# Performance work log

Hardware: AMD Instinct MI355X
Metric: run time of the kernel (lower is better)

Reference implementation:

```python
import jax, jax.numpy as jnp
import numpy as np

N = 50000      # nodes
E = 600000     # edges (avg degree 12)
D = 128        # in_dim == hidden_dim
H = 4          # heads
HD = 32        # per-head dim (hidden_dim // heads)
NEG = 0.2      # GATv2 leaky_relu negative slope (PyG default)
EPS = 1e-5     # LayerNorm eps


def setup_inputs() -> dict:
    key = jax.random.key(0)
    ks = jax.random.split(key, 4)
    inp = {
        "x": jax.random.normal(ks[0], (N, D), jnp.float32),
        "edge_index": jax.random.randint(ks[1], (2, E), 0, N, dtype=jnp.int32),
    }
    glorot = 1.0 / np.sqrt(D)
    for i in range(2):
        k = jax.random.split(jax.random.fold_in(ks[2], i), 8)
        inp[f"Wl{i}"] = jax.random.normal(k[0], (D, H * HD), jnp.float32) * glorot
        inp[f"bl{i}"] = jnp.zeros((H * HD,), jnp.float32)
        inp[f"Wr{i}"] = jax.random.normal(k[1], (D, H * HD), jnp.float32) * glorot
        inp[f"br{i}"] = jnp.zeros((H * HD,), jnp.float32)
        inp[f"att{i}"] = jax.random.normal(k[2], (H, HD), jnp.float32) * (1.0 / np.sqrt(HD))
        inp[f"bias{i}"] = jnp.zeros((H * HD,), jnp.float32)
        inp[f"g{i}"] = jnp.ones((H * HD,), jnp.float32)   # LayerNorm gamma
        inp[f"b{i}"] = jnp.zeros((H * HD,), jnp.float32)  # LayerNorm beta
    return inp


def _gat_layer(h, src, dst, Wl, bl, Wr, br, att, bias, g, b):
    # GATv2: x_l from source nodes, x_r from destination nodes
    xl = (h @ Wl + bl).reshape(N, H, HD)
    xr = (h @ Wr + br).reshape(N, H, HD)
    # edge-wise attention score: att . leaky_relu(x_l[j] + x_r[i])
    e = jax.nn.leaky_relu(xl[src] + xr[dst], NEG)          # [E, H, HD]
    score = jnp.einsum('ehd,hd->eh', e, att)               # [E, H]
    # segment softmax over edges sharing a destination
    m = jax.ops.segment_max(score, dst, num_segments=N)    # [N, H]
    m = jnp.where(jnp.isfinite(m), m, 0.0)                 # isolated nodes
    ex = jnp.exp(score - m[dst])
    den = jax.ops.segment_sum(ex, dst, num_segments=N)
    alpha = ex / (den[dst] + 1e-16)                        # [E, H]
    # scatter-add aggregation of source messages
    out = jax.ops.segment_sum(alpha[:, :, None] * xl[src], dst, num_segments=N)
    out = out.reshape(N, H * HD) + bias
    # LayerNorm + ELU (dropout is identity in eval mode)
    mu = out.mean(-1, keepdims=True)
    var = out.var(-1, keepdims=True)
    out = (out - mu) / jnp.sqrt(var + EPS) * g + b
    return jax.nn.elu(out)


def reference(x, edge_index, Wl0, bl0, Wr0, br0, att0, bias0, g0, b0,
              Wl1, bl1, Wr1, br1, att1, bias1, g1, b1):
    src, dst = edge_index[0], edge_index[1]
    h = _gat_layer(x, src, dst, Wl0, bl0, Wr0, br0, att0, bias0, g0, b0)
    h = _gat_layer(h, src, dst, Wl1, bl1, Wr1, br1, att1, bias1, g1, b1)
    return h
```

## Files before the change

### kernel.cpp

```cpp
#include <hip/hip_runtime.h>

#define NN 50000
#define NN_PAD 50016
#define NE 600000
#define DD 128
#define NH 4
#define RB_CNT 3125
#define RB_PAD 3128

#define SCAN_T 512
#define SCAN_B ((NN + SCAN_T - 1) / SCAN_T)

#define LOG2E 1.44269504088896340736f

typedef short s16x8 __attribute__((ext_vector_type(8)));
typedef float f32x4 __attribute__((ext_vector_type(4)));

__device__ __forceinline__ unsigned short bfh(float f) {
  unsigned u = __float_as_uint(f);
  return (unsigned short)((u + 0x7fffu + ((u >> 16) & 1u)) >> 16);
}
__device__ __forceinline__ float bff(unsigned short h) {
  return __uint_as_float(((unsigned)h) << 16);
}

template <int CTRL>
__device__ __forceinline__ float dpp_add(float x) {
  int y = __builtin_amdgcn_update_dpp(0, __float_as_int(x), CTRL, 0xf, 0xf, true);
  return x + __int_as_float(y);
}

__global__ void zero_deg(int* __restrict__ deg) {
  int i = (blockIdx.x * 256 + threadIdx.x) << 2;
  if (i < NN) {
    int4 z = make_int4(0, 0, 0, 0);
    if (i + 3 < NN) *(int4*)(deg + i) = z;
    else for (int k = i; k < NN; k++) deg[k] = 0;
  }
}

__global__ void count_deg(const int* __restrict__ ei, int* __restrict__ deg) {
  int e = blockIdx.x * 256 + threadIdx.x;
  if (e < NE) atomicAdd(deg + ei[NE + e], 1);
}

__global__ __launch_bounds__(SCAN_T) void scan_partial(
    const int* __restrict__ deg, int* __restrict__ rowp, int* __restrict__ bsum) {
  __shared__ int buf[SCAN_T];
  int b = blockIdx.x, t = threadIdx.x;
  int i = b * SCAN_T + t;
  int v = (i < NN) ? deg[i] : 0;
  buf[t] = v;
  __syncthreads();
  for (int o = 1; o < SCAN_T; o <<= 1) {
    int add = (t >= o) ? buf[t - o] : 0;
    __syncthreads();
    buf[t] += add;
    __syncthreads();
  }
  if (i < NN) rowp[i] = buf[t] - v;
  if (t == SCAN_T - 1) bsum[b] = buf[t];
}

__global__ __launch_bounds__(SCAN_T) void scan_finish(
    const int* __restrict__ bsum, int* __restrict__ rowp, int* __restrict__ cur) {
  __shared__ int sb[SCAN_T];
  int b = blockIdx.x, t = threadIdx.x;
  int v = (t < SCAN_B) ? bsum[t] : 0;
  sb[t] = v;
  __syncthreads();
  for (int o = 1; o < SCAN_T; o <<= 1) {
    int add = (t >= o) ? sb[t - o] : 0;
    __syncthreads();
    sb[t] += add;
    __syncthreads();
  }
  int boff = sb[b] - bsum[b];
  int i = b * SCAN_T + t;
  if (i < NN) {
    int r = rowp[i] + boff;
    rowp[i] = r;
    cur[i] = r;
  }
  if (b == 0 && t == 0) rowp[NN] = sb[SCAN_B - 1];
}

__global__ void scatter_src(const int* __restrict__ ei,
                            int* __restrict__ cur, int* __restrict__ colsrc) {
  int e = blockIdx.x * 256 + threadIdx.x;
  if (e < NE) {
    int d = ei[NE + e];
    int p = atomicAdd(cur + d, 1);
    colsrc[p] = ei[e] << 8;
  }
}

__global__ __launch_bounds__(256) void prep_all(
    const float* __restrict__ h,
    const float* __restrict__ Wl0, const float* __restrict__ Wr0,
    const float* __restrict__ Wl1, const float* __restrict__ Wr1,
    unsigned short* __restrict__ Ah, unsigned short* __restrict__ Am,
    unsigned short* __restrict__ Bh, unsigned short* __restrict__ Bm) {
  int b = blockIdx.x;
  if (b < RB_CNT) {
    int tid = b * 256 + threadIdx.x;
    int lr = tid & 15;
    int g = (tid >> 4) & 3;
    int kt = (tid >> 6) & 3;
    int rb = tid >> 8;
    int row = rb * 16 + lr;
    const float* p = h + (size_t)row * DD + kt * 32 + 4 * g;
    float4 f0 = *(const float4*)(p);
    float4 f1 = *(const float4*)(p + 16);
    float fs[8] = {f0.x, f0.y, f0.z, f0.w, f1.x, f1.y, f1.z, f1.w};
    s16x8 hi, mid;
#pragma unroll
    for (int e = 0; e < 8; e++) {
      unsigned short hh = bfh(fs[e]);
      hi[e] = (short)hh;
      mid[e] = (short)bfh(fs[e] - bff(hh));
    }
    *(s16x8*)(Ah + (size_t)tid * 8) = hi;
    *(s16x8*)(Am + (size_t)tid * 8) = mid;
  } else {
    int tid = (b - RB_CNT) * 256 + threadIdx.x;
    int lay = tid >> 12;
    int t = tid & 4095;
    int lr = t & 15;
    int g = (t >> 4) & 3;
    int kt = (t >> 6) & 3;
    int ct = t >> 8;
    int col = ct * 16 + lr;
    const float* W = (col < DD) ? (lay ? Wl1 : Wl0) : (lay ? Wr1 : Wr0);
    int cc = (col < DD) ? col : col - DD;
    s16x8 hi, mid;
#pragma unroll
    for (int e = 0; e < 8; e++) {
      int k = kt * 32 + ((e >> 2) << 4) + 4 * g + (e & 3);
      float w = W[(size_t)k * DD + cc];
      unsigned short hh = bfh(w);
      hi[e] = (short)hh;
      mid[e] = (short)bfh(w - bff(hh));
    }
    *(s16x8*)(Bh + (size_t)tid * 8) = hi;
    *(s16x8*)(Bm + (size_t)tid * 8) = mid;
  }
}

__global__ __launch_bounds__(256, 3) void dual_gemm_mfma(
    const unsigned short* __restrict__ Ah, const unsigned short* __restrict__ Am,
    const unsigned short* __restrict__ Bh, const unsigned short* __restrict__ Bm,
    const float* __restrict__ blv, const float* __restrict__ brv,
    unsigned short* __restrict__ xlb, unsigned short* __restrict__ xrb) {
  const int tid = threadIdx.x;
  const int lane = tid & 63;
  const int wv = tid >> 6;
  const int lr = lane & 15;
  const int g = lane >> 4;
  const int rb0 = blockIdx.x * 2;

  f32x4 acc[2][4];
#pragma unroll
  for (int rt = 0; rt < 2; rt++)
#pragma unroll
    for (int nt = 0; nt < 4; nt++)
#pragma unroll
      for (int e = 0; e < 4; e++) acc[rt][nt][e] = 0.f;

#pragma unroll
  for (int kt = 0; kt < 4; kt++) {
    s16x8 ah[2], am[2], bh[4], bm[4];
#pragma unroll
    for (int rt = 0; rt < 2; rt++) {
      size_t off = ((((size_t)((rb0 + rt) * 4 + kt)) * 4 + g) * 16 + lr) * 8;
      ah[rt] = *(const s16x8*)(Ah + off);
      am[rt] = *(const s16x8*)(Am + off);
    }
#pragma unroll
    for (int nt = 0; nt < 4; nt++) {
      int ct = wv * 4 + nt;
      size_t off = ((((size_t)(ct * 4 + kt)) * 4 + g) * 16 + lr) * 8;
      bh[nt] = *(const s16x8*)(Bh + off);
      bm[nt] = *(const s16x8*)(Bm + off);
    }
#pragma unroll
    for (int rt = 0; rt < 2; rt++)
#pragma unroll
      for (int nt = 0; nt < 4; nt++) {
        acc[rt][nt] = __builtin_amdgcn_mfma_f32_16x16x32_bf16(ah[rt], bh[nt], acc[rt][nt], 0, 0, 0);
        acc[rt][nt] = __builtin_amdgcn_mfma_f32_16x16x32_bf16(ah[rt], bm[nt], acc[rt][nt], 0, 0, 0);
        acc[rt][nt] = __builtin_amdgcn_mfma_f32_16x16x32_bf16(am[rt], bh[nt], acc[rt][nt], 0, 0, 0);
      }
  }

#pragma unroll
  for (int nt = 0; nt < 4; nt++) {
    int col = wv * 64 + nt * 16 + lr;
    unsigned short* dst = (col < DD) ? (xlb + col) : (xrb + (col - DD));
    float bv = (col < DD) ? blv[col] : brv[col - DD];
#pragma unroll
    for (int rt = 0; rt < 2; rt++) {
      int rowb = blockIdx.x * 32 + rt * 16 + 4 * g;
#pragma unroll
      for (int r = 0; r < 4; r++)
        dst[(size_t)(rowb + r) * DD] = bfh(acc[rt][nt][r] + bv);
    }
  }
}

template <int SPLIT>
__global__ __launch_bounds__(256) void fused_edge_agg(
    const int* __restrict__ rowp, const int* __restrict__ colsrc,
    const unsigned short* __restrict__ xlb, const unsigned short* __restrict__ xrb,
    const float* __restrict__ att, const float* __restrict__ bias,
    const float* __restrict__ gam, const float* __restrict__ bet,
    float* __restrict__ out, unsigned short* __restrict__ Oh,
    unsigned short* __restrict__ Om) {
  int node = (blockIdx.x * 256 + threadIdx.x) >> 5;
  if (node >= NN) return;
  int il = threadIdx.x & 31;
  int d0 = il << 2;

  ushort4 xru = *(const ushort4*)(xrb + (size_t)node * DD + d0);
  float4 xrv; xrv.x = bff(xru.x); xrv.y = bff(xru.y);
  xrv.z = bff(xru.z); xrv.w = bff(xru.w);
  float4 atv = *(const float4*)(att + d0);
  atv.x *= LOG2E; atv.y *= LOG2E; atv.z *= LOG2E; atv.w *= LOG2E;
  int j0 = rowp[node];
  int j1 = rowp[node + 1];

  float den = 0.f;
  float a0 = 0.f, a1 = 0.f, a2 = 0.f, a3 = 0.f;
  const char* xlb8 = (const char*)xlb;
  const int goff = il << 3;

  for (int j = j0; j < j1; j += 4) {
    bool v1 = (j + 1) < j1, v2 = (j + 2) < j1, v3 = (j + 3) < j1;
    int s0 = colsrc[j];
    int s1 = colsrc[v1 ? j + 1 : j];
    int s2 = colsrc[v2 ? j + 2 : j];
    int s3 = colsrc[v3 ? j + 3 : j];
    ushort4 g0 = *(const ushort4*)(xlb8 + (size_t)(unsigned)(s0 + goff));
    ushort4 g1 = *(const ushort4*)(xlb8 + (size_t)(unsigned)(s1 + goff));
    ushort4 g2 = *(const ushort4*)(xlb8 + (size_t)(unsigned)(s2 + goff));
    ushort4 g3 = *(const ushort4*)(xlb8 + (size_t)(unsigned)(s3 + goff));
    float x00 = bff(g0.x), x01 = bff(g0.y), x02 = bff(g0.z), x03 = bff(g0.w);
    float x10 = bff(g1.x), x11 = bff(g1.y), x12 = bff(g1.z), x13 = bff(g1.w);
    float x20 = bff(g2.x), x21 = bff(g2.y), x22 = bff(g2.z), x23 = bff(g2.w);
    float x30 = bff(g3.x), x31 = bff(g3.y), x32 = bff(g3.z), x33 = bff(g3.w);

    float t0, t1, t2, t3;
    t0 = x00 + xrv.x; t1 = x01 + xrv.y; t2 = x02 + xrv.z; t3 = x03 + xrv.w;
    t0 = fmaxf(t0, 0.2f * t0); t1 = fmaxf(t1, 0.2f * t1);
    t2 = fmaxf(t2, 0.2f * t2); t3 = fmaxf(t3, 0.2f * t3);
    float p0 = (t0 * atv.x + t1 * atv.y) + (t2 * atv.z + t3 * atv.w);
    t0 = x10 + xrv.x; t1 = x11 + xrv.y; t2 = x12 + xrv.z; t3 = x13 + xrv.w;
    t0 = fmaxf(t0, 0.2f * t0); t1 = fmaxf(t1, 0.2f * t1);
    t2 = fmaxf(t2, 0.2f * t2); t3 = fmaxf(t3, 0.2f * t3);
    float p1 = (t0 * atv.x + t1 * atv.y) + (t2 * atv.z + t3 * atv.w);
    t0 = x20 + xrv.x; t1 = x21 + xrv.y; t2 = x22 + xrv.z; t3 = x23 + xrv.w;
    t0 = fmaxf(t0, 0.2f * t0); t1 = fmaxf(t1, 0.2f * t1);
    t2 = fmaxf(t2, 0.2f * t2); t3 = fmaxf(t3, 0.2f * t3);
    float p2 = (t0 * atv.x + t1 * atv.y) + (t2 * atv.z + t3 * atv.w);
    t0 = x30 + xrv.x; t1 = x31 + xrv.y; t2 = x32 + xrv.z; t3 = x33 + xrv.w;
    t0 = fmaxf(t0, 0.2f * t0); t1 = fmaxf(t1, 0.2f * t1);
    t2 = fmaxf(t2, 0.2f * t2); t3 = fmaxf(t3, 0.2f * t3);
    float p3 = (t0 * atv.x + t1 * atv.y) + (t2 * atv.z + t3 * atv.w);

    p0 = dpp_add<0xB1>(p0);  p1 = dpp_add<0xB1>(p1);
    p2 = dpp_add<0xB1>(p2);  p3 = dpp_add<0xB1>(p3);
    p0 = dpp_add<0x4E>(p0);  p1 = dpp_add<0x4E>(p1);
    p2 = dpp_add<0x4E>(p2);  p3 = dpp_add<0x4E>(p3);
    p0 = dpp_add<0x141>(p0); p1 = dpp_add<0x141>(p1);
    p2 = dpp_add<0x141>(p2); p3 = dpp_add<0x141>(p3);

    float w0 = exp2f(p0);
    float w1 = v1 ? exp2f(p1) : 0.f;
    float w2 = v2 ? exp2f(p2) : 0.f;
    float w3 = v3 ? exp2f(p3) : 0.f;
    den += (w0 + w1) + (w2 + w3);
    a0 += (w0 * x00 + w1 * x10) + (w2 * x20 + w3 * x30);
    a1 += (w0 * x01 + w1 * x11) + (w2 * x21 + w3 * x31);
    a2 += (w0 * x02 + w1 * x12) + (w2 * x22 + w3 * x32);
    a3 += (w0 * x03 + w1 * x13) + (w2 * x23 + w3 * x33);
  }

  float inv = 1.f / (den + 1e-16f);
  float4 bi = *(const float4*)(bias + d0);
  float vx0 = a0 * inv + bi.x, vx1 = a1 * inv + bi.y;
  float vx2 = a2 * inv + bi.z, vx3 = a3 * inv + bi.w;

  float s1 = (vx0 + vx1) + (vx2 + vx3);
  float s2 = (vx0 * vx0 + vx1 * vx1) + (vx2 * vx2 + vx3 * vx3);
  s1 = dpp_add<0xB1>(s1);  s2 = dpp_add<0xB1>(s2);
  s1 = dpp_add<0x4E>(s1);  s2 = dpp_add<0x4E>(s2);
  s1 = dpp_add<0x124>(s1); s2 = dpp_add<0x124>(s2);
  s1 = dpp_add<0x128>(s1); s2 = dpp_add<0x128>(s2);
  s1 += __shfl_xor(s1, 16); s2 += __shfl_xor(s2, 16);
  float mean = s1 * (1.f / 128.f);
  float var = s2 * (1.f / 128.f) - mean * mean;
  float rstd = rsqrtf(var + 1e-5f);
  float4 gm = *(const float4*)(gam + d0);
  float4 bt = *(const float4*)(bet + d0);
  float n0 = (vx0 - mean) * rstd * gm.x + bt.x;
  float n1 = (vx1 - mean) * rstd * gm.y + bt.y;
  float n2 = (vx2 - mean) * rstd * gm.z + bt.z;
  float n3 = (vx3 - mean) * rstd * gm.w + bt.w;
  n0 = n0 > 0.f ? n0 : expf(n0) - 1.f;
  n1 = n1 > 0.f ? n1 : expf(n1) - 1.f;
  n2 = n2 > 0.f ? n2 : expf(n2) - 1.f;
  n3 = n3 > 0.f ? n3 : expf(n3) - 1.f;

  if (SPLIT) {
    int rb = node >> 4, lr16 = node & 15;
    int kt = d0 >> 5;
    int g = (d0 & 15) >> 2;
    int e0 = ((d0 >> 4) & 1) << 2;
    size_t off = ((((size_t)(rb * 4 + kt)) * 4 + g) * 16 + lr16) * 8 + e0;
    unsigned short h0 = bfh(n0), h1 = bfh(n1), h2 = bfh(n2), h3 = bfh(n3);
    ushort4 hv; hv.x = h0; hv.y = h1; hv.z = h2; hv.w = h3;
    ushort4 mv;
    mv.x = bfh(n0 - bff(h0)); mv.y = bfh(n1 - bff(h1));
    mv.z = bfh(n2 - bff(h2)); mv.w = bfh(n3 - bff(h3));
    *(ushort4*)(Oh + off) = hv;
    *(ushort4*)(Om + off) = mv;
  } else {
    float4 o; o.x = n0; o.y = n1; o.z = n2; o.w = n3;
    *(float4*)(out + (size_t)node * DD + d0) = o;
  }
}

extern "C" void kernel_launch(void* const* d_in, const int* in_sizes, int n_in,
                              void* d_out, int out_size, void* d_ws, size_t ws_size,
                              hipStream_t stream) {
  const float* x  = (const float*)d_in[0];
  const int*   ei = (const int*)d_in[1];
  const float* Wl[2]   = {(const float*)d_in[2],  (const float*)d_in[10]};
  const float* bl[2]   = {(const float*)d_in[3],  (const float*)d_in[11]};
  const float* Wr[2]   = {(const float*)d_in[4],  (const float*)d_in[12]};
  const float* br[2]   = {(const float*)d_in[5],  (const float*)d_in[13]};
  const float* att[2]  = {(const float*)d_in[6],  (const float*)d_in[14]};
  const float* bias[2] = {(const float*)d_in[7],  (const float*)d_in[15]};
  const float* gam[2]  = {(const float*)d_in[8],  (const float*)d_in[16]};
  const float* bet[2]  = {(const float*)d_in[9],  (const float*)d_in[17]};
  float* out = (float*)d_out;

  char* w = (char*)d_ws;
  auto carve = [&](size_t bytes) {
    char* p = w;
    w += (bytes + 255) & ~(size_t)255;
    return p;
  };
  unsigned short* xlb = (unsigned short*)carve((size_t)NN_PAD * DD * 2);
  unsigned short* xrb = (unsigned short*)carve((size_t)NN_PAD * DD * 2);
  int*   deg    = (int*)carve((size_t)NN * 4);
  int*   cur    = (int*)carve((size_t)NN * 4);
  int*   rowp   = (int*)carve((size_t)(NN + 1) * 4);
  int*   colsrc = (int*)carve((size_t)NE * 4);
  int*   bsum   = (int*)carve((size_t)SCAN_B * 4);
  unsigned short* Ah = (unsigned short*)carve((size_t)RB_PAD * 2048 * 2);
  unsigned short* Am = (unsigned short*)carve((size_t)RB_PAD * 2048 * 2);
  unsigned short* Bh = (unsigned short*)carve((size_t)8192 * 8 * 2);
  unsigned short* Bm = (unsigned short*)carve((size_t)8192 * 8 * 2);

  zero_deg<<<(NN / 4 + 255) / 256, 256, 0, stream>>>(deg);
  count_deg<<<(NE + 255) / 256, 256, 0, stream>>>(ei, deg);
  scan_partial<<<SCAN_B, SCAN_T, 0, stream>>>(deg, rowp, bsum);
  scan_finish<<<SCAN_B, SCAN_T, 0, stream>>>(bsum, rowp, cur);
  scatter_src<<<(NE + 255) / 256, 256, 0, stream>>>(ei, cur, colsrc);

  prep_all<<<RB_CNT + 32, 256, 0, stream>>>(x, Wl[0], Wr[0], Wl[1], Wr[1],
                                            Ah, Am, Bh, Bm);

  for (int l = 0; l < 2; l++) {
    dual_gemm_mfma<<<(NN + 31) / 32, 256, 0, stream>>>(
        Ah, Am, Bh + (size_t)l * 4096 * 8, Bm + (size_t)l * 4096 * 8,
        bl[l], br[l], xlb, xrb);
    if (l == 0) {
      fused_edge_agg<1><<<(NN * 32 + 255) / 256, 256, 0, stream>>>(
          rowp, colsrc, xlb, xrb, att[l], bias[l], gam[l], bet[l], out, Ah, Am);
    } else {
      fused_edge_agg<0><<<(NN * 32 + 255) / 256, 256, 0, stream>>>(
          rowp, colsrc, xlb, xrb, att[l], bias[l], gam[l], bet[l], out, Ah, Am);
    }
  }
}
```

Measured before the change: 194.3 us.

## Merge setup kernels into fused launches and prefetch next edge indices

Folds degree zeroing into the prep kernel and runs the edge-degree count inside the layer-0 GEMM launch as extra blocks, so fewer launches are needed and the independent work can overlap. The edge aggregation loop now loads the next four source indices while the current gathers are processed, software-pipelining the index load against the feature gather. The cost is some extra register pressure in the aggregation kernel. The GEMM kernel's launch bounds now also apply to the atomic count blocks.

Measured after the change: 183.9 us. 5.4% less time.

```diff
diff --git a/kernel.cpp b/kernel.cpp
--- a/kernel.cpp
+++ b/kernel.cpp
@@ -7,6 +7,9 @@
 #define NH 4
 #define RB_CNT 3125
 #define RB_PAD 3128
+#define GEMM_BLKS ((NN + 31) / 32)
+#define COUNT_BLKS ((NE + 255) / 256)
+#define ZERO_BLKS ((NN / 4 + 255) / 256)
 
 #define SCAN_T 512
 #define SCAN_B ((NN + SCAN_T - 1) / SCAN_T)
@@ -30,18 +33,158 @@
   return x + __int_as_float(y);
 }
 
-__global__ void zero_deg(int* __restrict__ deg) {
-  int i = (blockIdx.x * 256 + threadIdx.x) << 2;
-  if (i < NN) {
-    int4 z = make_int4(0, 0, 0, 0);
-    if (i + 3 < NN) *(int4*)(deg + i) = z;
-    else for (int k = i; k < NN; k++) deg[k] = 0;
-  }
-}
-
-__global__ void count_deg(const int* __restrict__ ei, int* __restrict__ deg) {
-  int e = blockIdx.x * 256 + threadIdx.x;
-  if (e < NE) atomicAdd(deg + ei[NE + e], 1);
+__device__ __forceinline__ void prep_a_body(
+    int tid, const float* __restrict__ h,
+    unsigned short* __restrict__ Ah, unsigned short* __restrict__ Am) {
+  int lr = tid & 15;
+  int g = (tid >> 4) & 3;
+  int kt = (tid >> 6) & 3;
+  int rb = tid >> 8;
+  int row = rb * 16 + lr;
+  const float* p = h + (size_t)row * DD + kt * 32 + 4 * g;
+  float4 f0 = *(const float4*)(p);
+  float4 f1 = *(const float4*)(p + 16);
+  float fs[8] = {f0.x, f0.y, f0.z, f0.w, f1.x, f1.y, f1.z, f1.w};
+  s16x8 hi, mid;
+#pragma unroll
+  for (int e = 0; e < 8; e++) {
+    unsigned short hh = bfh(fs[e]);
+    hi[e] = (short)hh;
+    mid[e] = (short)bfh(fs[e] - bff(hh));
+  }
+  *(s16x8*)(Ah + (size_t)tid * 8) = hi;
+  *(s16x8*)(Am + (size_t)tid * 8) = mid;
+}
+
+__device__ __forceinline__ void prep_w_body(
+    int tid, const float* __restrict__ Wl0, const float* __restrict__ Wr0,
+    const float* __restrict__ Wl1, const float* __restrict__ Wr1,
+    unsigned short* __restrict__ Bh, unsigned short* __restrict__ Bm) {
+  int lay = tid >> 12;
+  int t = tid & 4095;
+  int lr = t & 15;
+  int g = (t >> 4) & 3;
+  int kt = (t >> 6) & 3;
+  int ct = t >> 8;
+  int col = ct * 16 + lr;
+  const float* W = (col < DD) ? (lay ? Wl1 : Wl0) : (lay ? Wr1 : Wr0);
+  int cc = (col < DD) ? col : col - DD;
+  s16x8 hi, mid;
+#pragma unroll
+  for (int e = 0; e < 8; e++) {
+    int k = kt * 32 + ((e >> 2) << 4) + 4 * g + (e & 3);
+    float w = W[(size_t)k * DD + cc];
+    unsigned short hh = bfh(w);
+    hi[e] = (short)hh;
+    mid[e] = (short)bfh(w - bff(hh));
+  }
+  *(s16x8*)(Bh + (size_t)tid * 8) = hi;
+  *(s16x8*)(Bm + (size_t)tid * 8) = mid;
+}
+
+__device__ __forceinline__ void gemm_body(
+    int bid, int tid,
+    const unsigned short* __restrict__ Ah, const unsigned short* __restrict__ Am,
+    const unsigned short* __restrict__ Bh, const unsigned short* __restrict__ Bm,
+    const float* __restrict__ blv, const float* __restrict__ brv,
+    unsigned short* __restrict__ xlb, unsigned short* __restrict__ xrb) {
+  const int lane = tid & 63;
+  const int wv = tid >> 6;
+  const int lr = lane & 15;
+  const int g = lane >> 4;
+  const int rb0 = bid * 2;
+
+  f32x4 acc[2][4];
+#pragma unroll
+  for (int rt = 0; rt < 2; rt++)
+#pragma unroll
+    for (int nt = 0; nt < 4; nt++)
+#pragma unroll
+      for (int e = 0; e < 4; e++) acc[rt][nt][e] = 0.f;
+
+#pragma unroll
+  for (int kt = 0; kt < 4; kt++) {
+    s16x8 ah[2], am[2], bh[4], bm[4];
+#pragma unroll
+    for (int rt = 0; rt < 2; rt++) {
+      size_t off = ((((size_t)((rb0 + rt) * 4 + kt)) * 4 + g) * 16 + lr) * 8;
+      ah[rt] = *(const s16x8*)(Ah + off);
+      am[rt] = *(const s16x8*)(Am + off);
+    }
+#pragma unroll
+    for (int nt = 0; nt < 4; nt++) {
+      int ct = wv * 4 + nt;
+      size_t off = ((((size_t)(ct * 4 + kt)) * 4 + g) * 16 + lr) * 8;
+      bh[nt] = *(const s16x8*)(Bh + off);
+      bm[nt] = *(const s16x8*)(Bm + off);
+    }
+#pragma unroll
+    for (int rt = 0; rt < 2; rt++)
+#pragma unroll
+      for (int nt = 0; nt < 4; nt++) {
+        acc[rt][nt] = __builtin_amdgcn_mfma_f32_16x16x32_bf16(ah[rt], bh[nt], acc[rt][nt], 0, 0, 0);
+        acc[rt][nt] = __builtin_amdgcn_mfma_f32_16x16x32_bf16(ah[rt], bm[nt], acc[rt][nt], 0, 0, 0);
+        acc[rt][nt] = __builtin_amdgcn_mfma_f32_16x16x32_bf16(am[rt], bh[nt], acc[rt][nt], 0, 0, 0);
+      }
+  }
+
+#pragma unroll
+  for (int nt = 0; nt < 4; nt++) {
+    int col = wv * 64 + nt * 16 + lr;
+    unsigned short* dst = (col < DD) ? (xlb + col) : (xrb + (col - DD));
+    float bv = (col < DD) ? blv[col] : brv[col - DD];
+#pragma unroll
+    for (int rt = 0; rt < 2; rt++) {
+      int rowb = bid * 32 + rt * 16 + 4 * g;
+#pragma unroll
+      for (int r = 0; r < 4; r++)
+        dst[(size_t)(rowb + r) * DD] = bfh(acc[rt][nt][r] + bv);
+    }
+  }
+}
+
+__global__ __launch_bounds__(256) void init_fused(
+    const float* __restrict__ h,
+    const float* __restrict__ Wl0, const float* __restrict__ Wr0,
+    const float* __restrict__ Wl1, const float* __restrict__ Wr1,
+    unsigned short* __restrict__ Ah, unsigned short* __restrict__ Am,
+    unsigned short* __restrict__ Bh, unsigned short* __restrict__ Bm,
+    int* __restrict__ deg) {
+  int b = blockIdx.x;
+  if (b < RB_CNT) {
+    prep_a_body(b * 256 + threadIdx.x, h, Ah, Am);
+  } else if (b < RB_CNT + 32) {
+    prep_w_body((b - RB_CNT) * 256 + threadIdx.x, Wl0, Wr0, Wl1, Wr1, Bh, Bm);
+  } else {
+    int i = ((b - RB_CNT - 32) * 256 + threadIdx.x) << 2;
+    if (i < NN) {
+      if (i + 3 < NN) *(int4*)(deg + i) = make_int4(0, 0, 0, 0);
+      else for (int k = i; k < NN; k++) deg[k] = 0;
+    }
+  }
+}
+
+__global__ __launch_bounds__(256, 3) void count_gemm_fused(
+    const unsigned short* __restrict__ Ah, const unsigned short* __restrict__ Am,
+    const unsigned short* __restrict__ Bh, const unsigned short* __restrict__ Bm,
+    const float* __restrict__ blv, const float* __restrict__ brv,
+    unsigned short* __restrict__ xlb, unsigned short* __restrict__ xrb,
+    const int* __restrict__ ei, int* __restrict__ deg) {
+  int b = blockIdx.x;
+  if (b < GEMM_BLKS) {
+    gemm_body(b, threadIdx.x, Ah, Am, Bh, Bm, blv, brv, xlb, xrb);
+  } else {
+    int e = (b - GEMM_BLKS) * 256 + threadIdx.x;
+    if (e < NE) atomicAdd(deg + ei[NE + e], 1);
+  }
+}
+
+__global__ __launch_bounds__(256, 3) void dual_gemm_mfma(
+    const unsigned short* __restrict__ Ah, const unsigned short* __restrict__ Am,
+    const unsigned short* __restrict__ Bh, const unsigned short* __restrict__ Bm,
+    const float* __restrict__ blv, const float* __restrict__ brv,
+    unsigned short* __restrict__ xlb, unsigned short* __restrict__ xrb) {
+  gemm_body(blockIdx.x, threadIdx.x, Ah, Am, Bh, Bm, blv, brv, xlb, xrb);
 }
 
 __global__ __launch_bounds__(SCAN_T) void scan_partial(
@@ -95,119 +238,6 @@
   }
 }
 
-__global__ __launch_bounds__(256) void prep_all(
-    const float* __restrict__ h,
-    const float* __restrict__ Wl0, const float* __restrict__ Wr0,
-    const float* __restrict__ Wl1, const float* __restrict__ Wr1,
-    unsigned short* __restrict__ Ah, unsigned short* __restrict__ Am,
-    unsigned short* __restrict__ Bh, unsigned short* __restrict__ Bm) {
-  int b = blockIdx.x;
-  if (b < RB_CNT) {
-    int tid = b * 256 + threadIdx.x;
-    int lr = tid & 15;
-    int g = (tid >> 4) & 3;
-    int kt = (tid >> 6) & 3;
-    int rb = tid >> 8;
-    int row = rb * 16 + lr;
-    const float* p = h + (size_t)row * DD + kt * 32 + 4 * g;
-    float4 f0 = *(const float4*)(p);
-    float4 f1 = *(const float4*)(p + 16);
-    float fs[8] = {f0.x, f0.y, f0.z, f0.w, f1.x, f1.y, f1.z, f1.w};
-    s16x8 hi, mid;
-#pragma unroll
-    for (int e = 0; e < 8; e++) {
-      unsigned short hh = bfh(fs[e]);
-      hi[e] = (short)hh;
-      mid[e] = (short)bfh(fs[e] - bff(hh));
-    }
-    *(s16x8*)(Ah + (size_t)tid * 8) = hi;
-    *(s16x8*)(Am + (size_t)tid * 8) = mid;
-  } else {
-    int tid = (b - RB_CNT) * 256 + threadIdx.x;
-    int lay = tid >> 12;
-    int t = tid & 4095;
-    int lr = t & 15;
-    int g = (t >> 4) & 3;
-    int kt = (t >> 6) & 3;
-    int ct = t >> 8;
-    int col = ct * 16 + lr;
-    const float* W = (col < DD) ? (lay ? Wl1 : Wl0) : (lay ? Wr1 : Wr0);
-    int cc = (col < DD) ? col : col - DD;
-    s16x8 hi, mid;
-#pragma unroll
-    for (int e = 0; e < 8; e++) {
-      int k = kt * 32 + ((e >> 2) << 4) + 4 * g + (e & 3);
-      float w = W[(size_t)k * DD + cc];
-      unsigned short hh = bfh(w);
-      hi[e] = (short)hh;
-      mid[e] = (short)bfh(w - bff(hh));
-    }
-    *(s16x8*)(Bh + (size_t)tid * 8) = hi;
-    *(s16x8*)(Bm + (size_t)tid * 8) = mid;
-  }
-}
-
-__global__ __launch_bounds__(256, 3) void dual_gemm_mfma(
-    const unsigned short* __restrict__ Ah, const unsigned short* __restrict__ Am,
-    const unsigned short* __restrict__ Bh, const unsigned short* __restrict__ Bm,
-    const float* __restrict__ blv, const float* __restrict__ brv,
-    unsigned short* __restrict__ xlb, unsigned short* __restrict__ xrb) {
-  const int tid = threadIdx.x;
-  const int lane = tid & 63;
-  const int wv = tid >> 6;
-  const int lr = lane & 15;
-  const int g = lane >> 4;
-  const int rb0 = blockIdx.x * 2;
-
-  f32x4 acc[2][4];
-#pragma unroll
-  for (int rt = 0; rt < 2; rt++)
-#pragma unroll
-    for (int nt = 0; nt < 4; nt++)
-#pragma unroll
-      for (int e = 0; e < 4; e++) acc[rt][nt][e] = 0.f;
-
-#pragma unroll
-  for (int kt = 0; kt < 4; kt++) {
-    s16x8 ah[2], am[2], bh[4], bm[4];
-#pragma unroll
-    for (int rt = 0; rt < 2; rt++) {
-      size_t off = ((((size_t)((rb0 + rt) * 4 + kt)) * 4 + g) * 16 + lr) * 8;
-      ah[rt] = *(const s16x8*)(Ah + off);
-      am[rt] = *(const s16x8*)(Am + off);
-    }
-#pragma unroll
-    for (int nt = 0; nt < 4; nt++) {
-      int ct = wv * 4 + nt;
-      size_t off = ((((size_t)(ct * 4 + kt)) * 4 + g) * 16 + lr) * 8;
-      bh[nt] = *(const s16x8*)(Bh + off);
-      bm[nt] = *(const s16x8*)(Bm + off);
-    }
-#pragma unroll
-    for (int rt = 0; rt < 2; rt++)
-#pragma unroll
-      for (int nt = 0; nt < 4; nt++) {
-        acc[rt][nt] = __builtin_amdgcn_mfma_f32_16x16x32_bf16(ah[rt], bh[nt], acc[rt][nt], 0, 0, 0);
-        acc[rt][nt] = __builtin_amdgcn_mfma_f32_16x16x32_bf16(ah[rt], bm[nt], acc[rt][nt], 0, 0, 0);
-        acc[rt][nt] = __builtin_amdgcn_mfma_f32_16x16x32_bf16(am[rt], bh[nt], acc[rt][nt], 0, 0, 0);
-      }
-  }
-
-#pragma unroll
-  for (int nt = 0; nt < 4; nt++) {
-    int col = wv * 64 + nt * 16 + lr;
-    unsigned short* dst = (col < DD) ? (xlb + col) : (xrb + (col - DD));
-    float bv = (col < DD) ? blv[col] : brv[col - DD];
-#pragma unroll
-    for (int rt = 0; rt < 2; rt++) {
-      int rowb = blockIdx.x * 32 + rt * 16 + 4 * g;
-#pragma unroll
-      for (int r = 0; r < 4; r++)
-        dst[(size_t)(rowb + r) * DD] = bfh(acc[rt][nt][r] + bv);
-    }
-  }
-}
-
 template <int SPLIT>
 __global__ __launch_bounds__(256) void fused_edge_agg(
     const int* __restrict__ rowp, const int* __restrict__ colsrc,
@@ -234,16 +264,26 @@
   const char* xlb8 = (const char*)xlb;
   const int goff = il << 3;
 
+  int s0 = 0, s1 = 0, s2 = 0, s3 = 0;
+  if (j0 < j1) {
+    s0 = colsrc[j0];
+    s1 = colsrc[(j0 + 1 < j1) ? j0 + 1 : j0];
+    s2 = colsrc[(j0 + 2 < j1) ? j0 + 2 : j0];
+    s3 = colsrc[(j0 + 3 < j1) ? j0 + 3 : j0];
+  }
+
   for (int j = j0; j < j1; j += 4) {
     bool v1 = (j + 1) < j1, v2 = (j + 2) < j1, v3 = (j + 3) < j1;
-    int s0 = colsrc[j];
-    int s1 = colsrc[v1 ? j + 1 : j];
-    int s2 = colsrc[v2 ? j + 2 : j];
-    int s3 = colsrc[v3 ? j + 3 : j];
     ushort4 g0 = *(const ushort4*)(xlb8 + (size_t)(unsigned)(s0 + goff));
     ushort4 g1 = *(const ushort4*)(xlb8 + (size_t)(unsigned)(s1 + goff));
     ushort4 g2 = *(const ushort4*)(xlb8 + (size_t)(unsigned)(s2 + goff));
     ushort4 g3 = *(const ushort4*)(xlb8 + (size_t)(unsigned)(s3 + goff));
+    int jn = j + 4;
+    int t0i = colsrc[(jn < j1) ? jn : j];
+    int t1i = colsrc[(jn + 1 < j1) ? jn + 1 : j];
+    int t2i = colsrc[(jn + 2 < j1) ? jn + 2 : j];
+    int t3i = colsrc[(jn + 3 < j1) ? jn + 3 : j];
+
     float x00 = bff(g0.x), x01 = bff(g0.y), x02 = bff(g0.z), x03 = bff(g0.w);
     float x10 = bff(g1.x), x11 = bff(g1.y), x12 = bff(g1.z), x13 = bff(g1.w);
     float x20 = bff(g2.x), x21 = bff(g2.y), x22 = bff(g2.z), x23 = bff(g2.w);
@@ -283,6 +323,8 @@
     a1 += (w0 * x01 + w1 * x11) + (w2 * x21 + w3 * x31);
     a2 += (w0 * x02 + w1 * x12) + (w2 * x22 + w3 * x32);
     a3 += (w0 * x03 + w1 * x13) + (w2 * x23 + w3 * x33);
+
+    s0 = t0i; s1 = t1i; s2 = t2i; s3 = t3i;
   }
 
   float inv = 1.f / (den + 1e-16f);
@@ -290,15 +332,15 @@
   float vx0 = a0 * inv + bi.x, vx1 = a1 * inv + bi.y;
   float vx2 = a2 * inv + bi.z, vx3 = a3 * inv + bi.w;
 
-  float s1 = (vx0 + vx1) + (vx2 + vx3);
-  float s2 = (vx0 * vx0 + vx1 * vx1) + (vx2 * vx2 + vx3 * vx3);
-  s1 = dpp_add<0xB1>(s1);  s2 = dpp_add<0xB1>(s2);
-  s1 = dpp_add<0x4E>(s1);  s2 = dpp_add<0x4E>(s2);
-  s1 = dpp_add<0x124>(s1); s2 = dpp_add<0x124>(s2);
-  s1 = dpp_add<0x128>(s1); s2 = dpp_add<0x128>(s2);
-  s1 += __shfl_xor(s1, 16); s2 += __shfl_xor(s2, 16);
-  float mean = s1 * (1.f / 128.f);
-  float var = s2 * (1.f / 128.f) - mean * mean;
+  float s1f = (vx0 + vx1) + (vx2 + vx3);
+  float s2f = (vx0 * vx0 + vx1 * vx1) + (vx2 * vx2 + vx3 * vx3);
+  s1f = dpp_add<0xB1>(s1f);  s2f = dpp_add<0xB1>(s2f);
+  s1f = dpp_add<0x4E>(s1f);  s2f = dpp_add<0x4E>(s2f);
+  s1f = dpp_add<0x124>(s1f); s2f = dpp_add<0x124>(s2f);
+  s1f = dpp_add<0x128>(s1f); s2f = dpp_add<0x128>(s2f);
+  s1f += __shfl_xor(s1f, 16); s2f += __shfl_xor(s2f, 16);
+  float mean = s1f * (1.f / 128.f);
+  float var = s2f * (1.f / 128.f) - mean * mean;
   float rstd = rsqrtf(var + 1e-5f);
   float4 gm = *(const float4*)(gam + d0);
   float4 bt = *(const float4*)(bet + d0);
@@ -363,25 +405,18 @@
   unsigned short* Bh = (unsigned short*)carve((size_t)8192 * 8 * 2);
   unsigned short* Bm = (unsigned short*)carve((size_t)8192 * 8 * 2);
 
-  zero_deg<<<(NN / 4 + 255) / 256, 256, 0, stream>>>(deg);
-  count_deg<<<(NE + 255) / 256, 256, 0, stream>>>(ei, deg);
+  init_fused<<<RB_CNT + 32 + ZERO_BLKS, 256, 0, stream>>>(
+      x, Wl[0], Wr[0], Wl[1], Wr[1], Ah, Am, Bh, Bm, deg);
+  count_gemm_fused<<<GEMM_BLKS + COUNT_BLKS, 256, 0, stream>>>(
+      Ah, Am, Bh, Bm, bl[0], br[0], xlb, xrb, ei, deg);
   scan_partial<<<SCAN_B, SCAN_T, 0, stream>>>(deg, rowp, bsum);
   scan_finish<<<SCAN_B, SCAN_T, 0, stream>>>(bsum, rowp, cur);
-  scatter_src<<<(NE + 255) / 256, 256, 0, stream>>>(ei, cur, colsrc);
-
-  prep_all<<<RB_CNT + 32, 256, 0, stream>>>(x, Wl[0], Wr[0], Wl[1], Wr[1],
-                                            Ah, Am, Bh, Bm);
-
-  for (int l = 0; l < 2; l++) {
-    dual_gemm_mfma<<<(NN + 31) / 32, 256, 0, stream>>>(
-        Ah, Am, Bh + (size_t)l * 4096 * 8, Bm + (size_t)l * 4096 * 8,
-        bl[l], br[l], xlb, xrb);
-    if (l == 0) {
-      fused_edge_agg<1><<<(NN * 32 + 255) / 256, 256, 0, stream>>>(
-          rowp, colsrc, xlb, xrb, att[l], bias[l], gam[l], bet[l], out, Ah, Am);
-    } else {
-      fused_edge_agg<0><<<(NN * 32 + 255) / 256, 256, 0, stream>>>(
-          rowp, colsrc, xlb, xrb, att[l], bias[l], gam[l], bet[l], out, Ah, Am);
-    }
-  }
-}
+  scatter_src<<<COUNT_BLKS, 256, 0, stream>>>(ei, cur, colsrc);
+  fused_edge_agg<1><<<(NN * 32 + 255) / 256, 256, 0, stream>>>(
+      rowp, colsrc, xlb, xrb, att[0], bias[0], gam[0], bet[0], out, Ah, Am);
+  dual_gemm_mfma<<<GEMM_BLKS, 256, 0, stream>>>(
+      Ah, Am, Bh + (size_t)4096 * 8, Bm + (size_t)4096 * 8,
+      bl[1], br[1], xlb, xrb);
+  fused_edge_agg<0><<<(NN * 32 + 255) / 256, 256, 0, stream>>>(
+      rowp, colsrc, xlb, xrb, att[1], bias[1], gam[1], bet[1], out, Ah, Am);
+}
```
